# Kernel optimization log

Hardware: AMD Instinct MI355X
Metric: run time of the kernel (lower is better)

Reference implementation:

```python
import jax, jax.numpy as jnp
import numpy as np

HIDDEN = 256
MSG = 256
N_CLASSES = 2


def _ggnn(x, adj, W_lin, b_lin, W_ih, b_ih, W_hh, b_hh, n_timesteps):
    # Append supernode: zero-embedding row to h, ones row + zeros col to adj.
    N = x.shape[0]
    h0 = jnp.concatenate([x, jnp.zeros((1, x.shape[1]), x.dtype)], axis=0)  # [N+1, H]
    A = jnp.concatenate([adj, jnp.ones((1, N), adj.dtype)], axis=0)         # [N+1, N]
    A = jnp.concatenate([A, jnp.zeros((N + 1, 1), adj.dtype)], axis=1)      # [N+1, N+1]

    def step(h, _):
        msgs = h @ W_lin.T + b_lin          # [N+1, MSG] linear projection
        m = A @ msgs                        # [N+1, MSG] message aggregation
        # GRUCell (PyTorch convention): gates order r, z, n
        gi = m @ W_ih.T + b_ih              # [N+1, 3H]
        gh = h @ W_hh.T + b_hh              # [N+1, 3H]
        ir, iz, inn = jnp.split(gi, 3, axis=-1)
        hr, hz, hn = jnp.split(gh, 3, axis=-1)
        r = jax.nn.sigmoid(ir + hr)
        z = jax.nn.sigmoid(iz + hz)
        n = jnp.tanh(inn + r * hn)
        h_new = (1.0 - z) * n + z * h
        return h_new, None

    h, _ = jax.lax.scan(step, h0, None, length=n_timesteps)
    return h


def setup_inputs() -> dict:
    key = jax.random.key(0)
    ks = jax.random.split(key, 12)
    N = 8000
    inp = {
        "b_x": jax.random.normal(ks[0], (N, HIDDEN), dtype=jnp.float32),
        "b_adj": (jax.random.uniform(ks[1], (N, N), dtype=jnp.float32) < 0.002).astype(jnp.float32),
        "a_x": jax.random.normal(ks[2], (N, HIDDEN), dtype=jnp.float32),
        "a_adj": (jax.random.uniform(ks[3], (N, N), dtype=jnp.float32) < 0.002).astype(jnp.float32),
        "W_lin": jax.random.normal(ks[4], (MSG, HIDDEN), dtype=jnp.float32) * 0.05,
        "b_lin": jnp.zeros((MSG,), dtype=jnp.float32),
        "W_ih": jax.random.normal(ks[5], (3 * HIDDEN, MSG), dtype=jnp.float32) * 0.05,
        "b_ih": jnp.zeros((3 * HIDDEN,), dtype=jnp.float32),
        "W_hh": jax.random.normal(ks[6], (3 * HIDDEN, HIDDEN), dtype=jnp.float32) * 0.05,
        "b_hh": jnp.zeros((3 * HIDDEN,), dtype=jnp.float32),
        "W_fc": jax.random.normal(ks[7], (N_CLASSES, 2 * HIDDEN), dtype=jnp.float32) * 0.05,
        "b_fc": jnp.zeros((N_CLASSES,), dtype=jnp.float32),
        "n_timesteps": 8,
    }
    return inp


def reference(b_x, b_adj, a_x, a_adj, W_lin, b_lin, W_ih, b_ih, W_hh, b_hh, W_fc, b_fc, n_timesteps):
    b_h = _ggnn(b_x, b_adj, W_lin, b_lin, W_ih, b_ih, W_hh, b_hh, n_timesteps)
    a_h = _ggnn(a_x, a_adj, W_lin, b_lin, W_ih, b_ih, W_hh, b_hh, n_timesteps)
    supernodes = jnp.concatenate([b_h[-1, :], a_h[-1, :]], axis=0)  # [2H]
    logits = supernodes @ W_fc.T + b_fc                              # [n_classes]
    return jax.nn.log_softmax(logits, axis=0)
```

## Files before the change

### kernel.cpp

```cpp
#include <hip/hip_runtime.h>
#include <hip/hip_bf16.h>
#include <math.h>

#define NNODES 8000
#define NP1    8001
#define H      256
#define CAP    64
#define TSTEPS 8
#define MTOT   (2*NP1)
#define MPAD   16128
#define NRB    (MPAD/32)

typedef __attribute__((ext_vector_type(8))) short short8;
typedef __attribute__((ext_vector_type(4))) float floatx4;

__device__ __forceinline__ float bl2f(unsigned short u) {
  union { unsigned int i; float f; } z; z.i = ((unsigned int)u) << 16; return z.f;
}
__device__ __forceinline__ unsigned short f2bl(float f) {
  __hip_bfloat16 b = __float2bfloat16(f);
  return *(unsigned short*)&b;
}
__device__ __forceinline__ float sigf(float x) { return 1.f / (1.f + __expf(-x)); }
__device__ __forceinline__ float tanhf_fast(float x) { return 2.f / (1.f + __expf(-2.f * x)) - 1.f; }

__global__ __launch_bounds__(256) void build_ell_kernel(
    const float* __restrict__ adj_b, const float* __restrict__ adj_a,
    int* __restrict__ counts, int* __restrict__ colidx)
{
  int w = threadIdx.x >> 6, l = threadIdx.x & 63;
  int b = blockIdx.x * 4 + w;
  int g = b >= NNODES;
  int row = b - g * NNODES;
  const float* adj = (g ? adj_a : adj_b) + (size_t)row * NNODES;
  unsigned long long lt = (1ull << l) - 1;
  int base = 0;
  int* dst = colidx + (size_t)b * CAP;

  #define SLOT(vec, u, colv) { \
    bool nz = (&vec.x)[u] != 0.f; \
    unsigned long long m = __ballot(nz); \
    if (nz) { int idx = base + (int)__popcll(m & lt); if (idx < CAP) dst[idx] = (colv); } \
    base += (int)__popcll(m); }
  #define GROUP(vec, cb) { \
    bool any4 = ((&vec.x)[0] != 0.f) | ((&vec.x)[1] != 0.f) | \
                ((&vec.x)[2] != 0.f) | ((&vec.x)[3] != 0.f); \
    if (__ballot(any4)) { \
      SLOT(vec, 0, (cb) + 0) SLOT(vec, 1, (cb) + 1) \
      SLOT(vec, 2, (cb) + 2) SLOT(vec, 3, (cb) + 3) } }

  for (int c0 = l * 4; c0 < NNODES; c0 += 1024) {
    int c1 = c0 + 256, c2 = c0 + 512, c3 = c0 + 768;
    bool p1 = c1 < NNODES, p2 = c2 < NNODES, p3 = c3 < NNODES;
    float4 v0 = *(const float4*)(adj + c0);
    float4 v1 = p1 ? *(const float4*)(adj + c1) : make_float4(0,0,0,0);
    float4 v2 = p2 ? *(const float4*)(adj + c2) : make_float4(0,0,0,0);
    float4 v3 = p3 ? *(const float4*)(adj + c3) : make_float4(0,0,0,0);
    GROUP(v0, c0) GROUP(v1, c1) GROUP(v2, c2) GROUP(v3, c3)
  }
  #undef GROUP
  #undef SLOT
  if (l == 0) counts[b] = base < CAP ? base : CAP;
}

__global__ __launch_bounds__(256) void degf_kernel(
    const int* __restrict__ counts, float* __restrict__ degf)
{
  int row = blockIdx.x * 256 + threadIdx.x;
  float d = 0.f;
  if (row < MTOT) {
    int g = row >= NP1;
    int r = row - g * NP1;
    if (r < NNODES) d = (float)counts[g * NNODES + r];
    else if (r == NNODES) d = (float)NNODES;
  }
  degf[row] = d;
}

__global__ __launch_bounds__(256) void weights_kernel(
    const float* __restrict__ Wih, const float* __restrict__ Wlin,
    const float* __restrict__ blin, const float* __restrict__ Whh,
    __hip_bfloat16* __restrict__ Wbig2, float* __restrict__ bc)
{
  __shared__ float srow[H];
  __shared__ float red[256];
  int p = blockIdx.x;
  int ct32 = p / 96, w96 = p - ct32 * 96;
  int gb = w96 >> 4, u = w96 & 15;
  int jj = gb >> 1, uh = gb & 1;
  int c = ct32 * 32 + uh * 16 + u;
  int gr = jj * 256 + c;
  int t = threadIdx.x;
  size_t ob = (size_t)p * 512;
  srow[t] = Wih[(size_t)gr * H + t];
  __syncthreads();
  float acc = 0.f;
  #pragma unroll 8
  for (int k = 0; k < H; ++k) acc += srow[k] * Wlin[(size_t)k * H + t];
  Wbig2[ob + t] = __float2bfloat16(acc);
  Wbig2[ob + 256 + t] = __float2bfloat16(Whh[(size_t)gr * H + t]);
  red[t] = srow[t] * blin[t];
  __syncthreads();
  for (int s = 128; s > 0; s >>= 1) { if (t < s) red[t] += red[t + s]; __syncthreads(); }
  if (t == 0) bc[gr] = red[0];
}

__global__ __launch_bounds__(256) void init_h_kernel(
    const float* __restrict__ bx, const float* __restrict__ ax,
    __hip_bfloat16* __restrict__ hbf, float* __restrict__ cs0)
{
  int b = blockIdx.x;
  int t = threadIdx.x;
  float l0 = 0.f, l1 = 0.f;
  for (int q = 0; q < 32; ++q) {
    int row = b * 32 + q;
    int g = row >= NP1;
    int r = row - g * NP1;
    float v = 0.f;
    if (r < NNODES) {
      v = (g ? ax : bx)[(size_t)r * H + t];
      if (g) l1 += v; else l0 += v;
    }
    hbf[(size_t)row * H + t] = __float2bfloat16(v);
  }
  if (l0 != 0.f) atomicAdd(&cs0[t], l0);
  if (l1 != 0.f) atomicAdd(&cs0[256 + t], l1);
}

__global__ __launch_bounds__(256) void spmm_kernel(
    const unsigned short* __restrict__ hbf, unsigned short* __restrict__ haggbf,
    const int* __restrict__ counts, const int* __restrict__ colidx,
    const float* __restrict__ cs)
{
  int w = threadIdx.x >> 6, l = threadIdx.x & 63;
  int b = blockIdx.x * 4 + w;
  if (b >= MTOT) return;
  int g = b >= NP1;
  int r = b - g * NP1;
  size_t outoff = (size_t)b * H + l * 4;
  if (r == NNODES) {
    float4 v = *(const float4*)&cs[g * H + l * 4];
    ushort4 o; o.x = f2bl(v.x); o.y = f2bl(v.y); o.z = f2bl(v.z); o.w = f2bl(v.w);
    *(ushort4*)(haggbf + outoff) = o;
    return;
  }
  int rb = g * NNODES + r;
  int cnt = counts[rb];
  const int* cols = colidx + (size_t)rb * CAP;
  const unsigned short* hg = hbf + (size_t)g * NP1 * H;
  float a0 = 0.f, a1 = 0.f, a2 = 0.f, a3 = 0.f;
  int k = 0;
  for (; k + 4 <= cnt; k += 4) {
    int c0 = cols[k], c1 = cols[k+1], c2 = cols[k+2], c3 = cols[k+3];
    uint2 x0 = *(const uint2*)(hg + (size_t)c0 * H + l * 4);
    uint2 x1 = *(const uint2*)(hg + (size_t)c1 * H + l * 4);
    uint2 x2 = *(const uint2*)(hg + (size_t)c2 * H + l * 4);
    uint2 x3 = *(const uint2*)(hg + (size_t)c3 * H + l * 4);
    a0 += bl2f(x0.x & 0xffff) + bl2f(x1.x & 0xffff) + bl2f(x2.x & 0xffff) + bl2f(x3.x & 0xffff);
    a1 += bl2f(x0.x >> 16)    + bl2f(x1.x >> 16)    + bl2f(x2.x >> 16)    + bl2f(x3.x >> 16);
    a2 += bl2f(x0.y & 0xffff) + bl2f(x1.y & 0xffff) + bl2f(x2.y & 0xffff) + bl2f(x3.y & 0xffff);
    a3 += bl2f(x0.y >> 16)    + bl2f(x1.y >> 16)    + bl2f(x2.y >> 16)    + bl2f(x3.y >> 16);
  }
  for (; k < cnt; ++k) {
    uint2 x = *(const uint2*)(hg + (size_t)cols[k] * H + l * 4);
    a0 += bl2f(x.x & 0xffff); a1 += bl2f(x.x >> 16);
    a2 += bl2f(x.y & 0xffff); a3 += bl2f(x.y >> 16);
  }
  ushort4 o; o.x = f2bl(a0); o.y = f2bl(a1); o.z = f2bl(a2); o.w = f2bl(a3);
  *(ushort4*)(haggbf + outoff) = o;
}

__global__ __launch_bounds__(256, 2) void fused_gemm_gru_kernel(
    const __hip_bfloat16* __restrict__ haggbf, const __hip_bfloat16* __restrict__ hin,
    const __hip_bfloat16* __restrict__ Wbig2, const float* __restrict__ degf,
    const float* __restrict__ bc, const float* __restrict__ bih,
    const float* __restrict__ bhh,
    __hip_bfloat16* __restrict__ hout, float* __restrict__ cs_next)
{
  __shared__ __align__(16) short lsA[256 * 64];
  __shared__ __align__(16) short lsB[96 * 64];
  int bidx = blockIdx.x;
  int ct = bidx >> 6;
  int m_i = bidx & 63;
  if (m_i >= 63) return;
  int m0 = m_i * 256;
  const short* Bbase = (const short*)Wbig2 + (size_t)ct * 96 * 512;
  const short* Ai = (const short*)haggbf;
  const short* Ah = (const short*)hin;
  const unsigned short* hin_us = (const unsigned short*)hin;
  int t = threadIdx.x;
  int w = t >> 6, l = t & 63;
  int lr = l >> 3;
  int lc = l & 7;
  int wm = (w & 1) * 128, uh = w >> 1;
  int q = l >> 4, lm = l & 15;
  floatx4 acc[8][4] = {};

  for (int ks = 0; ks < 8; ++ks) {
    int k0 = ks * 64;
    bool ihalf = ks < 4;
    const short* Asrc = ihalf ? Ai : Ah;
    int ka = k0 & 255;
    #pragma unroll
    for (int j = 0; j < 8; ++j) {
      int r = w * 64 + j * 8 + lr;
      int sc = lc ^ (r & 7);
      const short* ga = Asrc + (size_t)(m0 + r) * H + ka + sc * 8;
      short* la = lsA + (w * 64 + j * 8) * 64;
      __builtin_amdgcn_global_load_lds((const __attribute__((address_space(1))) void*)ga,
                                       (__attribute__((address_space(3))) void*)la, 16, 0, 0);
    }
    #pragma unroll
    for (int j = 0; j < 3; ++j) {
      int r = w * 24 + j * 8 + lr;
      int sc = lc ^ (r & 7);
      const short* gb = Bbase + (size_t)r * 512 + k0 + sc * 8;
      short* lb = lsB + (w * 24 + j * 8) * 64;
      __builtin_amdgcn_global_load_lds((const __attribute__((address_space(1))) void*)gb,
                                       (__attribute__((address_space(3))) void*)lb, 16, 0, 0);
    }
    __syncthreads();
    #pragma unroll
    for (int kh = 0; kh < 2; ++kh) {
      int kc = kh * 4 + q;
      short8 bfr[3];
      #pragma unroll
      for (int jj = 0; jj < 3; ++jj) {
        int n = (jj * 2 + uh) * 16 + lm;
        bfr[jj] = *(const short8*)&lsB[n * 64 + (kc ^ (n & 7)) * 8];
      }
      #pragma unroll
      for (int i = 0; i < 8; ++i) {
        int m = wm + i * 16 + lm;
        short8 af = *(const short8*)&lsA[m * 64 + (kc ^ (m & 7)) * 8];
        acc[i][0] = __builtin_amdgcn_mfma_f32_16x16x32_bf16(af, bfr[0], acc[i][0], 0, 0, 0);
        acc[i][1] = __builtin_amdgcn_mfma_f32_16x16x32_bf16(af, bfr[1], acc[i][1], 0, 0, 0);
        if (ihalf)
          acc[i][2] = __builtin_amdgcn_mfma_f32_16x16x32_bf16(af, bfr[2], acc[i][2], 0, 0, 0);
        else
          acc[i][3] = __builtin_amdgcn_mfma_f32_16x16x32_bf16(af, bfr[2], acc[i][3], 0, 0, 0);
      }
    }
    __syncthreads();
  }

  int c = ct * 32 + uh * 16 + lm;
  float bcr = bc[c], bcz = bc[256 + c], bcn = bc[512 + c];
  float br  = bih[c] + bhh[c];
  float bz  = bih[256 + c] + bhh[256 + c];
  float bin = bih[512 + c];
  float bhn = bhh[512 + c];
  float lu0 = 0.f, lu1 = 0.f;
  #pragma unroll
  for (int i = 0; i < 8; ++i) {
    int row0 = m0 + wm + i * 16 + q * 4;
    float4 dg = *(const float4*)&degf[row0];
    #pragma unroll
    for (int reg = 0; reg < 4; ++reg) {
      int row = row0 + reg;
      float deg = (&dg.x)[reg];
      float rg = sigf(acc[i][0][reg] + deg * bcr + br);
      float z  = sigf(acc[i][1][reg] + deg * bcz + bz);
      float n  = tanhf_fast(acc[i][2][reg] + deg * bcn + bin + rg * (acc[i][3][reg] + bhn));
      size_t hoff = (size_t)row * H + c;
      float hp = bl2f(hin_us[hoff]);
      float hnew = (1.f - z) * n + z * hp;
      hout[hoff] = __float2bfloat16(hnew);
      if (row < NP1) { if (row < NNODES) lu0 += hnew; }
      else { if (row - NP1 < NNODES) lu1 += hnew; }
    }
  }
  lu0 += __shfl_down(lu0, 32); lu0 += __shfl_down(lu0, 16);
  lu1 += __shfl_down(lu1, 32); lu1 += __shfl_down(lu1, 16);
  if (q == 0) {
    if (lu0 != 0.f) atomicAdd(&cs_next[c], lu0);
    if (lu1 != 0.f) atomicAdd(&cs_next[256 + c], lu1);
  }
}

__global__ __launch_bounds__(256) void final_kernel(
    const unsigned short* __restrict__ hbf, const float* __restrict__ Wfc,
    const float* __restrict__ bfc, float* __restrict__ out)
{
  __shared__ float red0[256];
  __shared__ float red1[256];
  int t = threadIdx.x;
  float sn0 = bl2f(hbf[(size_t)NNODES * H + t]);
  float sn1 = bl2f(hbf[((size_t)NP1 + NNODES) * H + t]);
  red0[t] = sn0 * Wfc[t]       + sn1 * Wfc[H + t];
  red1[t] = sn0 * Wfc[512 + t] + sn1 * Wfc[512 + H + t];
  __syncthreads();
  for (int s = 128; s > 0; s >>= 1) {
    if (t < s) { red0[t] += red0[t + s]; red1[t] += red1[t + s]; }
    __syncthreads();
  }
  if (t == 0) {
    float l0 = red0[0] + bfc[0], l1 = red1[0] + bfc[1];
    float m = fmaxf(l0, l1);
    float lse = m + logf(expf(l0 - m) + expf(l1 - m));
    out[0] = l0 - lse;
    out[1] = l1 - lse;
  }
}

extern "C" void kernel_launch(void* const* d_in, const int* in_sizes, int n_in,
                              void* d_out, int out_size, void* d_ws, size_t ws_size,
                              hipStream_t stream) {
  const float* b_x   = (const float*)d_in[0];
  const float* b_adj = (const float*)d_in[1];
  const float* a_x   = (const float*)d_in[2];
  const float* a_adj = (const float*)d_in[3];
  const float* Wlin  = (const float*)d_in[4];
  const float* blin  = (const float*)d_in[5];
  const float* Wih   = (const float*)d_in[6];
  const float* bih   = (const float*)d_in[7];
  const float* Whh   = (const float*)d_in[8];
  const float* bhh   = (const float*)d_in[9];
  const float* Wfc   = (const float*)d_in[10];
  const float* bfc   = (const float*)d_in[11];
  float* out = (float*)d_out;

  char* ws = (char*)d_ws;
  size_t off = 0;
  auto alloc = [&](size_t bytes) {
    void* p = ws + off;
    off += (bytes + 255) & ~(size_t)255;
    return p;
  };
  __hip_bfloat16* hbf0   = (__hip_bfloat16*)alloc((size_t)MPAD * H * 2);
  __hip_bfloat16* hbf1   = (__hip_bfloat16*)alloc((size_t)MPAD * H * 2);
  __hip_bfloat16* haggbf = (__hip_bfloat16*)alloc((size_t)MPAD * H * 2);
  __hip_bfloat16* Wbig2  = (__hip_bfloat16*)alloc((size_t)768 * 512 * 2);
  float* bc              = (float*)alloc((size_t)768 * 4);
  int* colidx            = (int*)alloc((size_t)2 * NNODES * CAP * 4);
  int* counts            = (int*)alloc((size_t)2 * NNODES * 4 + 1024);
  float* degf            = (float*)alloc((size_t)MPAD * 4);
  float* cs              = (float*)alloc((size_t)(TSTEPS + 1) * 2 * H * 4);

  hipMemsetAsync(cs, 0, (size_t)(TSTEPS + 1) * 2 * H * 4, stream);

  build_ell_kernel<<<4000, 256, 0, stream>>>(b_adj, a_adj, counts, colidx);
  degf_kernel<<<MPAD / 256, 256, 0, stream>>>(counts, degf);
  weights_kernel<<<768, 256, 0, stream>>>(Wih, Wlin, blin, Whh, Wbig2, bc);
  init_h_kernel<<<NRB, 256, 0, stream>>>(b_x, a_x, hbf0, cs);

  __hip_bfloat16* ping[2] = { hbf0, hbf1 };
  for (int t = 0; t < TSTEPS; ++t) {
    __hip_bfloat16* hin  = ping[t & 1];
    __hip_bfloat16* hout = ping[(t + 1) & 1];
    spmm_kernel<<<(MTOT + 3) / 4, 256, 0, stream>>>(
        (const unsigned short*)hin, (unsigned short*)haggbf, counts, colidx, cs + t * 2 * H);
    fused_gemm_gru_kernel<<<512, 256, 0, stream>>>(
        haggbf, hin, Wbig2, degf, bc, bih, bhh, hout, cs + (t + 1) * 2 * H);
  }
  final_kernel<<<1, 256, 0, stream>>>((const unsigned short*)ping[TSTEPS & 1], Wfc, bfc, out);
}
```

Baseline: 886.6 us.

## Restructure ELL build loop and remap spmm blocks to interleave graphs

```diff
diff --git a/kernel.cpp b/kernel.cpp
--- a/kernel.cpp
+++ b/kernel.cpp
@@ -37,29 +37,25 @@
   int base = 0;
   int* dst = colidx + (size_t)b * CAP;
 
-  #define SLOT(vec, u, colv) { \
-    bool nz = (&vec.x)[u] != 0.f; \
-    unsigned long long m = __ballot(nz); \
-    if (nz) { int idx = base + (int)__popcll(m & lt); if (idx < CAP) dst[idx] = (colv); } \
-    base += (int)__popcll(m); }
-  #define GROUP(vec, cb) { \
-    bool any4 = ((&vec.x)[0] != 0.f) | ((&vec.x)[1] != 0.f) | \
-                ((&vec.x)[2] != 0.f) | ((&vec.x)[3] != 0.f); \
-    if (__ballot(any4)) { \
-      SLOT(vec, 0, (cb) + 0) SLOT(vec, 1, (cb) + 1) \
-      SLOT(vec, 2, (cb) + 2) SLOT(vec, 3, (cb) + 3) } }
-
-  for (int c0 = l * 4; c0 < NNODES; c0 += 1024) {
-    int c1 = c0 + 256, c2 = c0 + 512, c3 = c0 + 768;
-    bool p1 = c1 < NNODES, p2 = c2 < NNODES, p3 = c3 < NNODES;
-    float4 v0 = *(const float4*)(adj + c0);
-    float4 v1 = p1 ? *(const float4*)(adj + c1) : make_float4(0,0,0,0);
-    float4 v2 = p2 ? *(const float4*)(adj + c2) : make_float4(0,0,0,0);
-    float4 v3 = p3 ? *(const float4*)(adj + c3) : make_float4(0,0,0,0);
-    GROUP(v0, c0) GROUP(v1, c1) GROUP(v2, c2) GROUP(v3, c3)
-  }
-  #undef GROUP
-  #undef SLOT
+  #pragma unroll 4
+  for (int it = 0; it < 32; ++it) {
+    int c0 = it * 256 + l * 4;
+    float4 v = (c0 < NNODES) ? *(const float4*)(adj + c0) : make_float4(0, 0, 0, 0);
+    bool nz0 = v.x != 0.f, nz1 = v.y != 0.f, nz2 = v.z != 0.f, nz3 = v.w != 0.f;
+    bool any = nz0 | nz1 | nz2 | nz3;
+    if (__ballot(any)) {
+      unsigned long long m0 = __ballot(nz0);
+      unsigned long long m1 = __ballot(nz1);
+      unsigned long long m2 = __ballot(nz2);
+      unsigned long long m3 = __ballot(nz3);
+      int t0 = (int)__popcll(m0), t1 = (int)__popcll(m1), t2 = (int)__popcll(m2);
+      if (nz0) { int i0 = base + (int)__popcll(m0 & lt);           if (i0 < CAP) dst[i0] = c0; }
+      if (nz1) { int i1 = base + t0 + (int)__popcll(m1 & lt);      if (i1 < CAP) dst[i1] = c0 + 1; }
+      if (nz2) { int i2 = base + t0 + t1 + (int)__popcll(m2 & lt); if (i2 < CAP) dst[i2] = c0 + 2; }
+      if (nz3) { int i3 = base + t0 + t1 + t2 + (int)__popcll(m3 & lt); if (i3 < CAP) dst[i3] = c0 + 3; }
+      base += t0 + t1 + t2 + (int)__popcll(m3);
+    }
+  }
   if (l == 0) counts[b] = base < CAP ? base : CAP;
 }
 
@@ -133,10 +129,12 @@
     const float* __restrict__ cs)
 {
   int w = threadIdx.x >> 6, l = threadIdx.x & 63;
-  int b = blockIdx.x * 4 + w;
-  if (b >= MTOT) return;
-  int g = b >= NP1;
-  int r = b - g * NP1;
+  int B = blockIdx.x;
+  int g = (B & 7) >= 4;
+  int j = (B >> 3) * 4 + (B & 3);
+  int r = j * 4 + w;
+  if (r > NNODES) return;
+  int b = g * NP1 + r;
   size_t outoff = (size_t)b * H + l * 4;
   if (r == NNODES) {
     float4 v = *(const float4*)&cs[g * H + l * 4];
@@ -348,7 +346,7 @@
   for (int t = 0; t < TSTEPS; ++t) {
     __hip_bfloat16* hin  = ping[t & 1];
     __hip_bfloat16* hout = ping[(t + 1) & 1];
-    spmm_kernel<<<(MTOT + 3) / 4, 256, 0, stream>>>(
+    spmm_kernel<<<4096, 256, 0, stream>>>(
         (const unsigned short*)hin, (unsigned short*)haggbf, counts, colidx, cs + t * 2 * H);
     fused_gemm_gru_kernel<<<512, 256, 0, stream>>>(
         haggbf, hin, Wbig2, degf, bc, bih, bhh, hout, cs + (t + 1) * 2 * H);
```

New measurement: 880.4 us (median of 2 runs). Within noise of the previous version (-0.7%).
